# Kernel optimization log

Hardware: AMD Instinct MI355X
Metric: run time of the kernel (lower is better)

Reference implementation:

```python
import jax, jax.numpy as jnp
import numpy as np

E, H_HEADS, WS = 512, 16, 8
HEAD_D = E // H_HEADS
LN_EPS = 1e-5


def layernorm(x, g, b):
    mu = jnp.mean(x, axis=-1, keepdims=True)
    var = jnp.mean((x - mu) ** 2, axis=-1, keepdims=True)
    return (x - mu) / jnp.sqrt(var + LN_EPS) * g + b


def setup_inputs() -> dict:
    key = jax.random.key(0)
    ks = jax.random.split(key, 10)
    s = 0.02
    return {
        "x": jax.random.normal(ks[0], (4, 4096, E), jnp.float32),
        "in_proj_w": jax.random.normal(ks[1], (3 * E, E), jnp.float32) * s,
        "in_proj_b": jnp.zeros((3 * E,), jnp.float32),
        "out_w": jax.random.normal(ks[2], (E, E), jnp.float32) * s,
        "out_b": jnp.zeros((E,), jnp.float32),
        "ln1_g": jnp.ones((E,), jnp.float32),
        "ln1_b": jnp.zeros((E,), jnp.float32),
        "w1": jax.random.normal(ks[3], (4 * E, E), jnp.float32) * s,
        "b1": jnp.zeros((4 * E,), jnp.float32),
        "w2": jax.random.normal(ks[4], (E, 4 * E), jnp.float32) * s,
        "b2": jnp.zeros((E,), jnp.float32),
        "ln2_g": jnp.ones((E,), jnp.float32),
        "ln2_b": jnp.zeros((E,), jnp.float32),
        "num_patches_h": 64,
        "num_patches_w": 64,
    }


def reference(x, in_proj_w, in_proj_b, out_w, out_b, ln1_g, ln1_b,
              w1, b1, w2, b2, ln2_g, ln2_b, num_patches_h, num_patches_w):
    B, P, _ = x.shape
    Hp, Wp = num_patches_h, num_patches_w  # 64 divisible by WS -> no padding branch
    nwh, nww = Hp // WS, Wp // WS
    # window partition: (B, Hp, Wp, E) -> (B*nW, WS*WS, E)
    xw = x.reshape(B, nwh, WS, nww, WS, E).transpose(0, 1, 3, 2, 4, 5)
    xw = xw.reshape(B * nwh * nww, WS * WS, E)
    # nn.MultiheadAttention default batch_first=False: axis0 is SEQ (L=B*nW),
    # axis1 is BATCH (N=WS*WS). Reproduce that literal semantics.
    L, N = xw.shape[0], xw.shape[1]
    qkv = xw @ in_proj_w.T + in_proj_b          # (L, N, 3E)
    q, k, v = jnp.split(qkv, 3, axis=-1)
    qh = q.reshape(L, N, H_HEADS, HEAD_D)
    kh = k.reshape(L, N, H_HEADS, HEAD_D)
    vh = v.reshape(L, N, H_HEADS, HEAD_D)
    scale = 1.0 / np.sqrt(HEAD_D)
    scores = jnp.einsum('lnhd,mnhd->nhlm', qh, kh) * scale  # (N, h, L, L)
    attn = jax.nn.softmax(scores, axis=-1)
    o = jnp.einsum('nhlm,mnhd->lnhd', attn, vh).reshape(L, N, E)
    attn_out = o @ out_w.T + out_b
    y = layernorm(xw + attn_out, ln1_g, ln1_b)
    ffn = jax.nn.gelu(y @ w1.T + b1, approximate=False) @ w2.T + b2
    y = layernorm(y + ffn, ln2_g, ln2_b)
    # window unpartition
    y = y.reshape(B, nwh, nww, WS, WS, E).transpose(0, 1, 3, 2, 4, 5)
    return y.reshape(B, Hp * Wp, E)[:, :P, :]
```

## Files before the change

kernel.cpp:

```cpp
#include <hip/hip_runtime.h>
#include <cmath>


typedef _Float16 half8 __attribute__((ext_vector_type(8)));
typedef _Float16 half4v __attribute__((ext_vector_type(4)));
typedef float f32x4 __attribute__((ext_vector_type(4)));

#define GLOBAL_AS(p) ((const __attribute__((address_space(1))) void*)(p))
#define LDS_AS(p) ((__attribute__((address_space(3))) void*)(p))

__device__ __forceinline__ void gload_lds16(const _Float16* g, _Float16* l) {
  __builtin_amdgcn_global_load_lds(GLOBAL_AS(g), LDS_AS(l), 16, 0, 0);
}

__device__ __forceinline__ float wave_sum(float v) {
#pragma unroll
  for (int off = 32; off > 0; off >>= 1) v += __shfl_xor(v, off, 64);
  return v;
}

__device__ __forceinline__ float gelu_fast(float x) {
  const float y = 1.5957691216057308f * (x + 0.044715f * x * x * x);
  const float e = __expf(y);
  const float t = 1.0f - 2.0f / (e + 1.0f);
  return 0.5f * x * (1.0f + t);
}

__global__ __launch_bounds__(256) void castw4_kernel(
    const float* __restrict__ s0, _Float16* __restrict__ d0,
    const float* __restrict__ s1, _Float16* __restrict__ d1,
    const float* __restrict__ s2, _Float16* __restrict__ d2,
    const float* __restrict__ s3, _Float16* __restrict__ d3) {
  int b = blockIdx.x;
  const float* s; _Float16* d;
  if (b < 768) { s = s0; d = d0; }
  else if (b < 1024) { s = s1; d = d1; b -= 768; }
  else if (b < 2048) { s = s2; d = d2; b -= 1024; }
  else { s = s3; d = d3; b -= 2048; }
  const int i = (b * 256 + threadIdx.x) * 4;
  const float4 v = *(const float4*)&s[i];
  half4v o;
  o[0] = (_Float16)v.x; o[1] = (_Float16)v.y; o[2] = (_Float16)v.z; o[3] = (_Float16)v.w;
  *(half4v*)&d[i] = o;
}

__global__ __launch_bounds__(256) void gather_x_kernel(const float* __restrict__ x,
                                                       _Float16* __restrict__ xw) {
  const int idx = blockIdx.x * 256 + threadIdx.x;
  const int t = idx >> 6;
  const int e0 = (idx & 63) << 3;
  const int l = t >> 6, n = t & 63;
  const int bb = l >> 6, wh = (l >> 3) & 7, ww = l & 7;
  const int pi = n >> 3, pj = n & 7;
  const int xrow = (bb * 4096 + (wh * 8 + pi) * 64 + (ww * 8 + pj)) * 512;
  const float4 a = *(const float4*)&x[xrow + e0];
  const float4 b = *(const float4*)&x[xrow + e0 + 4];
  half8 o;
  o[0] = (_Float16)a.x; o[1] = (_Float16)a.y; o[2] = (_Float16)a.z; o[3] = (_Float16)a.w;
  o[4] = (_Float16)b.x; o[5] = (_Float16)b.y; o[6] = (_Float16)b.z; o[7] = (_Float16)b.w;
  *(half8*)&xw[t * 512 + e0] = o;
}

template <int EPI, int K, int BN>
__global__ __launch_bounds__(256, 4) void gemml_kernel(
    const _Float16* __restrict__ A, const _Float16* __restrict__ B,
    const float* __restrict__ bias, _Float16* __restrict__ C, int N) {
  constexpr int NT = K / 64;
  constexpr int TA = 128 * 64;
  constexpr int TB = BN * 64;
  constexpr int MREP = (BN == 128) ? 4 : 2;
  __shared__ _Float16 L[TA + TB];

  const int tid = threadIdx.x, lane = tid & 63, wave = tid >> 6;
  const int wr = (BN == 128) ? (wave >> 1) : wave;
  const int wc = (BN == 128) ? (wave & 1) : 0;
  const int lr = lane & 15, g = lane >> 4;

  const int nbn = N / BN;
  const int cpx = gridDim.x >> 3;
  const int wg = (blockIdx.x & 7) * cpx + (blockIdx.x >> 3);
  const int bm = wg / nbn, bn = wg % nbn;

  const int scol = ((lane & 7) ^ (lane >> 3)) << 3;
  const int srow = lane >> 3;
  const _Float16* aS = A + (size_t)(bm * 128 + wave * 8 + srow) * K + scol;
  const _Float16* bS = B + (size_t)(bn * BN + wave * 8 + srow) * K + scol;

  const int sw0 = ((g ^ (lr & 7)) << 3);
  const int sw1 = (((4 + g) ^ (lr & 7)) << 3);
  int arow[MREP], brow[4];
#pragma unroll
  for (int m = 0; m < MREP; ++m) arow[m] = (wr * (MREP * 16) + m * 16 + lr) * 64;
#pragma unroll
  for (int n = 0; n < 4; ++n) brow[n] = TA + (wc * 64 + n * 16 + lr) * 64;

  f32x4 acc[MREP][4] = {};

  for (int t = 0; t < NT; ++t) {
    const int koff = t * 64;
#pragma unroll
    for (int i = 0; i < 4; ++i)
      gload_lds16(aS + (size_t)(i * 32) * K + koff, &L[(i * 32 + wave * 8) * 64]);
#pragma unroll
    for (int i = 0; i < BN / 32; ++i)
      gload_lds16(bS + (size_t)(i * 32) * K + koff, &L[TA + (i * 32 + wave * 8) * 64]);
    __syncthreads();
    half8 af[MREP], bf[4];
#pragma unroll
    for (int m = 0; m < MREP; ++m) af[m] = *(const half8*)&L[arow[m] + sw0];
#pragma unroll
    for (int n = 0; n < 4; ++n) bf[n] = *(const half8*)&L[brow[n] + sw0];
    __builtin_amdgcn_s_setprio(1);
#pragma unroll
    for (int m = 0; m < MREP; ++m)
#pragma unroll
      for (int n = 0; n < 4; ++n)
        acc[m][n] = __builtin_amdgcn_mfma_f32_16x16x32_f16(af[m], bf[n], acc[m][n], 0, 0, 0);
    __builtin_amdgcn_s_setprio(0);
#pragma unroll
    for (int m = 0; m < MREP; ++m) af[m] = *(const half8*)&L[arow[m] + sw1];
#pragma unroll
    for (int n = 0; n < 4; ++n) bf[n] = *(const half8*)&L[brow[n] + sw1];
    __builtin_amdgcn_s_setprio(1);
#pragma unroll
    for (int m = 0; m < MREP; ++m)
#pragma unroll
      for (int n = 0; n < 4; ++n)
        acc[m][n] = __builtin_amdgcn_mfma_f32_16x16x32_f16(af[m], bf[n], acc[m][n], 0, 0, 0);
    __builtin_amdgcn_s_setprio(0);
    __syncthreads();
  }

  float bsv[4];
#pragma unroll
  for (int n = 0; n < 4; ++n) bsv[n] = bias[bn * BN + wc * 64 + n * 16 + lr];
  _Float16* Lc = &L[0] + wave * (MREP * 16 * 64);
#pragma unroll
  for (int m = 0; m < MREP; ++m)
#pragma unroll
    for (int n = 0; n < 4; ++n)
#pragma unroll
      for (int r = 0; r < 4; ++r) {
        float v = acc[m][n][r] + bsv[n];
        if (EPI == 1) v = gelu_fast(v);
        const int row = m * 16 + g * 4 + r;
        const int col = n * 16 + lr;
        Lc[row * 64 + (col ^ ((row & 7) << 3))] = (_Float16)v;
      }
  asm volatile("s_waitcnt lgkmcnt(0)" ::: "memory");
  const int rrow = lane >> 3, slot = lane & 7;
  const int growb = bm * 128 + wr * (MREP * 16);
  const int gcol = bn * BN + wc * 64 + slot * 8;
#pragma unroll
  for (int blk = 0; blk < MREP * 2; ++blk) {
    const int row = blk * 8 + rrow;
    const half8 vv = *(const half8*)&Lc[row * 64 + ((slot ^ (row & 7)) << 3)];
    *(half8*)&C[(size_t)(growb + row) * N + gcol] = vv;
  }
}

__global__ __launch_bounds__(256) void attn_kernel(const _Float16* __restrict__ qkv,
                                                   _Float16* __restrict__ o_out) {
  const int n = blockIdx.x & 63;
  const int h = blockIdx.x >> 6;
  __shared__ _Float16 Ksh[256 * 40];
  __shared__ _Float16 Vt[32 * 264];
  __shared__ _Float16 Pw[4 * 64 * 72];
  const int tid = threadIdx.x;
  const int wq = tid >> 6, lane = tid & 63;
  const int lr = lane & 15, g = lane >> 4;
  const int hq = h * 32;

#pragma unroll
  for (int pass = 0; pass < 4; ++pass) {
    const int e = pass * 2048 + tid * 8;
    const int m = e >> 5, d = e & 31;
    const int base = (m * 64 + n) * 1536 + hq;
    const half8 k8 = *(const half8*)&qkv[base + 512 + d];
    const half8 v8 = *(const half8*)&qkv[base + 1024 + d];
    *(half8*)&Ksh[m * 40 + d] = k8;
#pragma unroll
    for (int j = 0; j < 8; ++j) Vt[(d + j) * 264 + m] = v8[j];
  }
  half8 qf[4];
#pragma unroll
  for (int qt = 0; qt < 4; ++qt) {
    const int qg = wq * 64 + qt * 16 + lr;
    qf[qt] = *(const half8*)&qkv[(qg * 64 + n) * 1536 + hq + g * 8];
  }
  __syncthreads();

  f32x4 o[4][2] = {};
  float den[4] = {0.f, 0.f, 0.f, 0.f};
  const float scale = 0.17677669529663687f;
  _Float16* P = &Pw[wq * (64 * 72)];

  for (int it = 0; it < 4; ++it) {
    const int k0 = it * 64;
#pragma unroll
    for (int qt = 0; qt < 4; ++qt) {
#pragma unroll
      for (int kt = 0; kt < 4; ++kt) {
        const half8 kf = *(const half8*)&Ksh[(k0 + kt * 16 + lr) * 40 + g * 8];
        const f32x4 z = {0.f, 0.f, 0.f, 0.f};
        f32x4 st = __builtin_amdgcn_mfma_f32_16x16x32_f16(kf, qf[qt], z, 0, 0, 0);
        const float p0 = __expf(st[0] * scale);
        const float p1 = __expf(st[1] * scale);
        const float p2 = __expf(st[2] * scale);
        const float p3 = __expf(st[3] * scale);
        den[qt] += (p0 + p1) + (p2 + p3);
        half4v w;
        w[0] = (_Float16)p0; w[1] = (_Float16)p1;
        w[2] = (_Float16)p2; w[3] = (_Float16)p3;
        *(half4v*)&P[(qt * 16 + lr) * 72 + kt * 16 + g * 4] = w;
      }
    }
    __syncthreads();
#pragma unroll
    for (int qt = 0; qt < 4; ++qt) {
#pragma unroll
      for (int ks = 0; ks < 2; ++ks) {
        const half8 pf = *(const half8*)&P[(qt * 16 + lr) * 72 + ks * 32 + g * 8];
#pragma unroll
        for (int dt = 0; dt < 2; ++dt) {
          const half8 vf = *(const half8*)&Vt[(dt * 16 + lr) * 264 + k0 + ks * 32 + g * 8];
          o[qt][dt] = __builtin_amdgcn_mfma_f32_16x16x32_f16(pf, vf, o[qt][dt], 0, 0, 0);
        }
      }
    }
    __syncthreads();
  }

#pragma unroll
  for (int qt = 0; qt < 4; ++qt) {
    float dq = den[qt];
    dq += __shfl_xor(dq, 16);
    dq += __shfl_xor(dq, 32);
    const float inv = 1.0f / dq;
#pragma unroll
    for (int r = 0; r < 4; ++r) {
      const float invr = __shfl(inv, g * 4 + r);
      const int qg = wq * 64 + qt * 16 + g * 4 + r;
      const int obase = (qg * 64 + n) * 512 + hq;
#pragma unroll
      for (int dt = 0; dt < 2; ++dt)
        o_out[obase + dt * 16 + lr] = (_Float16)(o[qt][dt][r] * invr);
    }
  }
}

template <int FINAL>
__global__ __launch_bounds__(256) void ln_kernel(
    const float* __restrict__ res32, const _Float16* __restrict__ res16,
    const _Float16* __restrict__ add16,
    const float* __restrict__ g, const float* __restrict__ b,
    float* __restrict__ out32, _Float16* __restrict__ out16) {
  const int t = blockIdx.x * 4 + (threadIdx.x >> 6);
  const int lane = threadIdx.x & 63;
  const int e0 = lane << 3;
  const int l = t >> 6, n = t & 63;
  const int bb = l >> 6, wh = (l >> 3) & 7, ww = l & 7;
  const int pi = n >> 3, pj = n & 7;
  const int xrow = (bb * 4096 + (wh * 8 + pi) * 64 + (ww * 8 + pj)) * 512;
  const int trow = t * 512;
  const half8 a8 = *(const half8*)&add16[trow + e0];
  float v[8];
  if (FINAL) {
    const half8 r8 = *(const half8*)&res16[trow + e0];
#pragma unroll
    for (int e = 0; e < 8; ++e) v[e] = (float)r8[e] + (float)a8[e];
  } else {
    const float4 ra = *(const float4*)&res32[xrow + e0];
    const float4 rb = *(const float4*)&res32[xrow + e0 + 4];
    v[0] = ra.x + (float)a8[0]; v[1] = ra.y + (float)a8[1];
    v[2] = ra.z + (float)a8[2]; v[3] = ra.w + (float)a8[3];
    v[4] = rb.x + (float)a8[4]; v[5] = rb.y + (float)a8[5];
    v[6] = rb.z + (float)a8[6]; v[7] = rb.w + (float)a8[7];
  }
  float sm = 0.f;
#pragma unroll
  for (int e = 0; e < 8; ++e) sm += v[e];
  sm = wave_sum(sm);
  const float mu = sm * (1.0f / 512.0f);
  float vs = 0.f;
#pragma unroll
  for (int e = 0; e < 8; ++e) { const float d = v[e] - mu; vs += d * d; }
  vs = wave_sum(vs);
  const float rstd = rsqrtf(vs * (1.0f / 512.0f) + 1e-5f);
  const float4 g1 = *(const float4*)&g[e0];
  const float4 g2 = *(const float4*)&g[e0 + 4];
  const float4 b1 = *(const float4*)&b[e0];
  const float4 b2 = *(const float4*)&b[e0 + 4];
  float y[8];
  y[0] = (v[0] - mu) * rstd * g1.x + b1.x; y[1] = (v[1] - mu) * rstd * g1.y + b1.y;
  y[2] = (v[2] - mu) * rstd * g1.z + b1.z; y[3] = (v[3] - mu) * rstd * g1.w + b1.w;
  y[4] = (v[4] - mu) * rstd * g2.x + b2.x; y[5] = (v[5] - mu) * rstd * g2.y + b2.y;
  y[6] = (v[6] - mu) * rstd * g2.z + b2.z; y[7] = (v[7] - mu) * rstd * g2.w + b2.w;
  if (FINAL) {
    *(float4*)&out32[xrow + e0] = make_float4(y[0], y[1], y[2], y[3]);
    *(float4*)&out32[xrow + e0 + 4] = make_float4(y[4], y[5], y[6], y[7]);
  } else {
    half8 o16;
#pragma unroll
    for (int e = 0; e < 8; ++e) o16[e] = (_Float16)y[e];
    *(half8*)&out16[trow + e0] = o16;
  }
}

extern "C" void kernel_launch(void* const* d_in, const int* in_sizes, int n_in,
                              void* d_out, int out_size, void* d_ws, size_t ws_size,
                              hipStream_t stream) {
  const float* x    = (const float*)d_in[0];
  const float* ipw  = (const float*)d_in[1];
  const float* ipb  = (const float*)d_in[2];
  const float* outw = (const float*)d_in[3];
  const float* outb = (const float*)d_in[4];
  const float* ln1g = (const float*)d_in[5];
  const float* ln1b = (const float*)d_in[6];
  const float* w1   = (const float*)d_in[7];
  const float* b1   = (const float*)d_in[8];
  const float* w2   = (const float*)d_in[9];
  const float* b2   = (const float*)d_in[10];
  const float* ln2g = (const float*)d_in[11];
  const float* ln2b = (const float*)d_in[12];
  float* out = (float*)d_out;
  char* ws = (char*)d_ws;

  _Float16* wqkv_h = (_Float16*)(ws + 0);
  _Float16* wout_h = (_Float16*)(ws + 1572864);
  _Float16* w1_h   = (_Float16*)(ws + 2097152);
  _Float16* w2_h   = (_Float16*)(ws + 4194304);
  _Float16* xw_h   = (_Float16*)(ws + 6291456);
  _Float16* qkv_h  = (_Float16*)(ws + 23068672);
  _Float16* attn_h = (_Float16*)(ws + 90177536);
  _Float16* ao_h   = (_Float16*)(ws + 106954752);
  _Float16* h_h = qkv_h;
  _Float16* f_h = attn_h;
  _Float16* y16 = xw_h;

  castw4_kernel<<<3072, 256, 0, stream>>>(ipw, wqkv_h, outw, wout_h, w1, w1_h, w2, w2_h);
  gather_x_kernel<<<4096, 256, 0, stream>>>(x, xw_h);
  gemml_kernel<0, 512, 128><<<1536, 256, 0, stream>>>(xw_h, wqkv_h, ipb, qkv_h, 1536);
  attn_kernel<<<1024, 256, 0, stream>>>(qkv_h, attn_h);
  gemml_kernel<0, 512, 64><<<1024, 256, 0, stream>>>(attn_h, wout_h, outb, ao_h, 512);
  ln_kernel<0><<<4096, 256, 0, stream>>>(x, nullptr, ao_h, ln1g, ln1b, nullptr, y16);
  gemml_kernel<1, 512, 128><<<2048, 256, 0, stream>>>(y16, w1_h, b1, h_h, 2048);
  gemml_kernel<0, 2048, 64><<<1024, 256, 0, stream>>>(h_h, w2_h, b2, f_h, 512);
  ln_kernel<1><<<4096, 256, 0, stream>>>(nullptr, y16, f_h, ln2g, ln2b, out, nullptr);
}
```

Before: 204.8 us.

## Add 64x64-tile GEMM for N=512 projections and merge gather with weight cast

Introduces a smaller 64x64-tile GEMM kernel used for the out-projection and FFN down-projection (N=512), doubling the grid to 2048 blocks to improve occupancy and wave balance across CUs. The weight cast and window-gather kernels are merged into a single launch to save one kernel launch. The smaller tile lowers data reuse per block and increases global/L2 traffic for A and B, especially for the K=2048 GEMM, and the new loop is single-buffered with two barriers per k-step.

```diff
diff --git a/kernel.cpp b/kernel.cpp
--- a/kernel.cpp
+++ b/kernel.cpp
@@ -26,12 +26,30 @@
   return 0.5f * x * (1.0f + t);
 }
 
-__global__ __launch_bounds__(256) void castw4_kernel(
+__global__ __launch_bounds__(256) void pre_kernel(
+    const float* __restrict__ x, _Float16* __restrict__ xw,
     const float* __restrict__ s0, _Float16* __restrict__ d0,
     const float* __restrict__ s1, _Float16* __restrict__ d1,
     const float* __restrict__ s2, _Float16* __restrict__ d2,
     const float* __restrict__ s3, _Float16* __restrict__ d3) {
   int b = blockIdx.x;
+  if (b < 4096) {
+    const int idx = b * 256 + threadIdx.x;
+    const int t = idx >> 6;
+    const int e0 = (idx & 63) << 3;
+    const int l = t >> 6, n = t & 63;
+    const int bb = l >> 6, wh = (l >> 3) & 7, ww = l & 7;
+    const int pi = n >> 3, pj = n & 7;
+    const int xrow = (bb * 4096 + (wh * 8 + pi) * 64 + (ww * 8 + pj)) * 512;
+    const float4 a = *(const float4*)&x[xrow + e0];
+    const float4 c = *(const float4*)&x[xrow + e0 + 4];
+    half8 o;
+    o[0] = (_Float16)a.x; o[1] = (_Float16)a.y; o[2] = (_Float16)a.z; o[3] = (_Float16)a.w;
+    o[4] = (_Float16)c.x; o[5] = (_Float16)c.y; o[6] = (_Float16)c.z; o[7] = (_Float16)c.w;
+    *(half8*)&xw[t * 512 + e0] = o;
+    return;
+  }
+  b -= 4096;
   const float* s; _Float16* d;
   if (b < 768) { s = s0; d = d0; }
   else if (b < 1024) { s = s1; d = d1; b -= 768; }
@@ -42,23 +60,6 @@
   half4v o;
   o[0] = (_Float16)v.x; o[1] = (_Float16)v.y; o[2] = (_Float16)v.z; o[3] = (_Float16)v.w;
   *(half4v*)&d[i] = o;
-}
-
-__global__ __launch_bounds__(256) void gather_x_kernel(const float* __restrict__ x,
-                                                       _Float16* __restrict__ xw) {
-  const int idx = blockIdx.x * 256 + threadIdx.x;
-  const int t = idx >> 6;
-  const int e0 = (idx & 63) << 3;
-  const int l = t >> 6, n = t & 63;
-  const int bb = l >> 6, wh = (l >> 3) & 7, ww = l & 7;
-  const int pi = n >> 3, pj = n & 7;
-  const int xrow = (bb * 4096 + (wh * 8 + pi) * 64 + (ww * 8 + pj)) * 512;
-  const float4 a = *(const float4*)&x[xrow + e0];
-  const float4 b = *(const float4*)&x[xrow + e0 + 4];
-  half8 o;
-  o[0] = (_Float16)a.x; o[1] = (_Float16)a.y; o[2] = (_Float16)a.z; o[3] = (_Float16)a.w;
-  o[4] = (_Float16)b.x; o[5] = (_Float16)b.y; o[6] = (_Float16)b.z; o[7] = (_Float16)b.w;
-  *(half8*)&xw[t * 512 + e0] = o;
 }
 
 template <int EPI, int K, int BN>
@@ -156,6 +157,99 @@
     const int row = blk * 8 + rrow;
     const half8 vv = *(const half8*)&Lc[row * 64 + ((slot ^ (row & 7)) << 3)];
     *(half8*)&C[(size_t)(growb + row) * N + gcol] = vv;
+  }
+}
+
+template <int EPI, int K>
+__global__ void gemms_kernel(
+    const _Float16* __restrict__ A, const _Float16* __restrict__ B,
+    const float* __restrict__ bias, _Float16* __restrict__ C, int N) {
+  constexpr int NT = K / 64;
+  constexpr int TA = 64 * 64;
+  __shared__ _Float16 L[2 * TA];
+
+  const int tid = threadIdx.x, lane = tid & 63, wave = tid >> 6;
+  const int wr = wave >> 1, wc = wave & 1;
+  const int lr = lane & 15, g = lane >> 4;
+
+  const int nbn = N >> 6;
+  const int cpx = gridDim.x >> 3;
+  const int wg = (blockIdx.x & 7) * cpx + (blockIdx.x >> 3);
+  const int bm = wg / nbn, bn = wg % nbn;
+
+  const int scol = ((lane & 7) ^ (lane >> 3)) << 3;
+  const int srow = lane >> 3;
+  const _Float16* aS = A + (size_t)(bm * 64 + wave * 8 + srow) * K + scol;
+  const _Float16* bS = B + (size_t)(bn * 64 + wave * 8 + srow) * K + scol;
+
+  const int sw0 = ((g ^ (lr & 7)) << 3);
+  const int sw1 = (((4 + g) ^ (lr & 7)) << 3);
+  int arow[2], brow[2];
+#pragma unroll
+  for (int m = 0; m < 2; ++m) arow[m] = (wr * 32 + m * 16 + lr) * 64;
+#pragma unroll
+  for (int n = 0; n < 2; ++n) brow[n] = TA + (wc * 32 + n * 16 + lr) * 64;
+
+  f32x4 acc[2][2] = {};
+
+  for (int t = 0; t < NT; ++t) {
+    const int koff = t * 64;
+#pragma unroll
+    for (int i = 0; i < 2; ++i)
+      gload_lds16(aS + (size_t)(i * 32) * K + koff, &L[(i * 32 + wave * 8) * 64]);
+#pragma unroll
+    for (int i = 0; i < 2; ++i)
+      gload_lds16(bS + (size_t)(i * 32) * K + koff, &L[TA + (i * 32 + wave * 8) * 64]);
+    __syncthreads();
+    half8 af[2], bf[2];
+#pragma unroll
+    for (int m = 0; m < 2; ++m) af[m] = *(const half8*)&L[arow[m] + sw0];
+#pragma unroll
+    for (int n = 0; n < 2; ++n) bf[n] = *(const half8*)&L[brow[n] + sw0];
+    __builtin_amdgcn_s_setprio(1);
+#pragma unroll
+    for (int m = 0; m < 2; ++m)
+#pragma unroll
+      for (int n = 0; n < 2; ++n)
+        acc[m][n] = __builtin_amdgcn_mfma_f32_16x16x32_f16(af[m], bf[n], acc[m][n], 0, 0, 0);
+    __builtin_amdgcn_s_setprio(0);
+#pragma unroll
+    for (int m = 0; m < 2; ++m) af[m] = *(const half8*)&L[arow[m] + sw1];
+#pragma unroll
+    for (int n = 0; n < 2; ++n) bf[n] = *(const half8*)&L[brow[n] + sw1];
+    __builtin_amdgcn_s_setprio(1);
+#pragma unroll
+    for (int m = 0; m < 2; ++m)
+#pragma unroll
+      for (int n = 0; n < 2; ++n)
+        acc[m][n] = __builtin_amdgcn_mfma_f32_16x16x32_f16(af[m], bf[n], acc[m][n], 0, 0, 0);
+    __builtin_amdgcn_s_setprio(0);
+    __syncthreads();
+  }
+
+  float bsv[2];
+#pragma unroll
+  for (int n = 0; n < 2; ++n) bsv[n] = bias[bn * 64 + wc * 32 + n * 16 + lr];
+#pragma unroll
+  for (int m = 0; m < 2; ++m)
+#pragma unroll
+    for (int n = 0; n < 2; ++n)
+#pragma unroll
+      for (int r = 0; r < 4; ++r) {
+        float v = acc[m][n][r] + bsv[n];
+        if (EPI == 1) v = gelu_fast(v);
+        const int row = wr * 32 + m * 16 + g * 4 + r;
+        const int col = wc * 32 + n * 16 + lr;
+        L[row * 64 + (col ^ ((row & 7) << 3))] = (_Float16)v;
+      }
+  __syncthreads();
+  const int slot = tid & 7;
+  const int gcol = bn * 64 + slot * 8;
+#pragma unroll
+  for (int rnd = 0; rnd < 2; ++rnd) {
+    const int row = rnd * 32 + (tid >> 3);
+    const half8 vv = *(const half8*)&L[row * 64 + ((slot ^ (row & 7)) << 3)];
+    *(half8*)&C[(size_t)(bm * 64 + row) * N + gcol] = vv;
   }
 }
 
@@ -338,13 +432,13 @@
   _Float16* f_h = attn_h;
   _Float16* y16 = xw_h;
 
-  castw4_kernel<<<3072, 256, 0, stream>>>(ipw, wqkv_h, outw, wout_h, w1, w1_h, w2, w2_h);
-  gather_x_kernel<<<4096, 256, 0, stream>>>(x, xw_h);
+  pre_kernel<<<7168, 256, 0, stream>>>(x, xw_h, ipw, wqkv_h, outw, wout_h,
+                                       w1, w1_h, w2, w2_h);
   gemml_kernel<0, 512, 128><<<1536, 256, 0, stream>>>(xw_h, wqkv_h, ipb, qkv_h, 1536);
   attn_kernel<<<1024, 256, 0, stream>>>(qkv_h, attn_h);
-  gemml_kernel<0, 512, 64><<<1024, 256, 0, stream>>>(attn_h, wout_h, outb, ao_h, 512);
+  gemms_kernel<0, 512><<<2048, 256, 0, stream>>>(attn_h, wout_h, outb, ao_h, 512);
   ln_kernel<0><<<4096, 256, 0, stream>>>(x, nullptr, ao_h, ln1g, ln1b, nullptr, y16);
   gemml_kernel<1, 512, 128><<<2048, 256, 0, stream>>>(y16, w1_h, b1, h_h, 2048);
-  gemml_kernel<0, 2048, 64><<<1024, 256, 0, stream>>>(h_h, w2_h, b2, f_h, 512);
+  gemms_kernel<0, 2048><<<2048, 256, 0, stream>>>(h_h, w2_h, b2, f_h, 512);
   ln_kernel<1><<<4096, 256, 0, stream>>>(nullptr, y16, f_h, ln2g, ln2b, out, nullptr);
 }
```

Result: slower. 211.8 us (+3.4%).
